# Performance work log

Measured on AMD Instinct MI355X. Metric: run time of the kernel, lower is better.

The kernel has to match this reference:

```python
import jax, jax.numpy as jnp
import numpy as np

N = 100000
E = 3200000
D_IN = 256
D_OUT = 256
K = 3


def setup_inputs() -> dict:
    key = jax.random.key(0)
    k1, k2, k3, k4, k5 = jax.random.split(key, 5)
    x = jax.random.normal(k1, (N, D_IN), dtype=jnp.float32)
    # xavier-uniform-ish weight
    lim = float(np.sqrt(6.0 / (D_IN + D_OUT)))
    weight = jax.random.uniform(k2, (D_IN, D_OUT), dtype=jnp.float32, minval=-lim, maxval=lim)
    bias = jnp.zeros((D_OUT,), dtype=jnp.float32)
    edge_weight = jax.random.uniform(k3, (E,), dtype=jnp.float32) / 32.0  # ~normalized adj values
    edge_row = jax.random.randint(k4, (E,), 0, N, dtype=jnp.int32)
    edge_col = jax.random.randint(k5, (E,), 0, N, dtype=jnp.int32)
    return {"x": x, "weight": weight, "bias": bias, "edge_weight": edge_weight,
            "edge_row": edge_row, "edge_col": edge_col}


def _spmm(edge_weight, edge_row, edge_col, support):
    # out[i] = sum_{e: row_e == i} w_e * support[col_e]
    msgs = edge_weight[:, None] * support[edge_col]  # [E, D]
    return jax.ops.segment_sum(msgs, edge_row, num_segments=N)


def reference(x, weight, bias, edge_weight, edge_row, edge_col):
    support = x @ weight            # [N, D_OUT]
    output = support
    for _ in range(K):
        support = _spmm(edge_weight, edge_row, edge_col, support)
        output = output + support
    return output + bias
```

## Files before the change

### kernel.cpp

```cpp
#include <hip/hip_runtime.h>

#define D 256
#define NB 196
#define RPB_SHIFT 9
#define CAP 20480
#define CHUNK 8192

typedef __attribute__((ext_vector_type(8))) short bf16x8;
typedef __attribute__((ext_vector_type(4))) float f32x4;
typedef __attribute__((ext_vector_type(2))) float f32x2;

__device__ __forceinline__ unsigned bf16rne(float f) {
    unsigned u = __float_as_uint(f);
    return (u + 0x7fffu + ((u >> 16) & 1u)) >> 16;
}
__device__ __forceinline__ unsigned char fp8enc(float f) {
    return (unsigned char)(__builtin_amdgcn_cvt_pk_fp8_f32(f, f, 0, false) & 0xFF);
}


__global__ __launch_bounds__(256) void cursor_init(int* __restrict__ g) {
    int t = threadIdx.x;
    g[t] = t * CAP;
}

__global__ __launch_bounds__(256) void partA(const int* __restrict__ erow,
                                             const int* __restrict__ ecol,
                                             const float* __restrict__ ew,
                                             int* __restrict__ gcur,
                                             int2* __restrict__ temp, int E) {
    __shared__ int2 rec[CHUNK];
    __shared__ unsigned char bkt[CHUNK];
    __shared__ int hist[256], sc[256], excl[256], cur[256], lbase[256];
    int t = threadIdx.x;
    int base = blockIdx.x * CHUNK;
    hist[t] = 0;
    __syncthreads();
    int rows[32];
    #pragma unroll
    for (int j = 0; j < 32; j++) {
        int e = base + t + 256 * j;
        rows[j] = (e < E) ? erow[e] : -1;
        if (rows[j] >= 0) atomicAdd(&hist[rows[j] >> RPB_SHIFT], 1);
    }
    __syncthreads();
    sc[t] = hist[t];
    __syncthreads();
    for (int off = 1; off < 256; off <<= 1) {
        int v = (t >= off) ? sc[t - off] : 0;
        __syncthreads();
        sc[t] += v;
        __syncthreads();
    }
    int ex = sc[t] - hist[t];
    excl[t] = ex;
    cur[t] = ex;
    lbase[t] = atomicAdd(&gcur[t], hist[t]);
    __syncthreads();
    int total = sc[255];
    #pragma unroll
    for (int j = 0; j < 32; j++) {
        if (rows[j] >= 0) {
            int e = base + t + 256 * j;
            int b = rows[j] >> RPB_SHIFT;
            int rl = rows[j] & 511;
            int p = atomicAdd(&cur[b], 1);
            int2 r;
            r.x = ecol[e] | (rl << 17);
            r.y = __float_as_int(ew[e]);
            rec[p] = r;
            bkt[p] = (unsigned char)b;
        }
    }
    __syncthreads();
    for (int i = t; i < total; i += 256) {
        int b = bkt[i];
        temp[(size_t)lbase[b] + (i - excl[b])] = rec[i];
    }
}

__global__ __launch_bounds__(256) void scanB(const int* __restrict__ gcur,
                                             int* __restrict__ bbase) {
    __shared__ int sc[256];
    int t = threadIdx.x;
    int c = (t < NB) ? (gcur[t] - t * CAP) : 0;
    sc[t] = c;
    __syncthreads();
    for (int off = 1; off < 256; off <<= 1) {
        int v = (t >= off) ? sc[t - off] : 0;
        __syncthreads();
        sc[t] += v;
        __syncthreads();
    }
    if (t < NB) bbase[t] = sc[t] - c;
}

__global__ __launch_bounds__(256) void partB(const int2* __restrict__ temp,
                                             const int* __restrict__ gcur,
                                             const int* __restrict__ bbase,
                                             int* __restrict__ row_ptr,
                                             int2* __restrict__ edges,
                                             int N, int E) {
    __shared__ int hist[512], excl[512], scp[256];
    int b = blockIdx.x;
    int t = threadIdx.x;
    int cnt = gcur[b] - b * CAP;
    int base = bbase[b];
    const int2* src = temp + (size_t)b * CAP;
    hist[t] = 0;
    hist[t + 256] = 0;
    __syncthreads();
    for (int i = t; i < cnt; i += 256)
        atomicAdd(&hist[(src[i].x >> 17) & 511], 1);
    __syncthreads();
    int v0 = hist[2 * t], v1 = hist[2 * t + 1];
    int ps = v0 + v1;
    scp[t] = ps;
    __syncthreads();
    for (int off = 1; off < 256; off <<= 1) {
        int v = (t >= off) ? scp[t - off] : 0;
        __syncthreads();
        scp[t] += v;
        __syncthreads();
    }
    int ep = scp[t] - ps;
    excl[2 * t] = ep;
    excl[2 * t + 1] = ep + v0;
    int r0 = (b << RPB_SHIFT) + 2 * t;
    if (r0 < N) row_ptr[r0] = base + ep;
    if (r0 + 1 < N) row_ptr[r0 + 1] = base + ep + v0;
    if (b == 0 && t == 0) row_ptr[N] = E;
    __syncthreads();
    for (int i = t; i < cnt; i += 256) {
        int2 r = src[i];
        int rl = (r.x >> 17) & 511;
        int p = base + atomicAdd(&excl[rl], 1);
        int2 o;
        o.x = r.x & 0x1FFFF;
        o.y = r.y;
        edges[p] = o;
    }
}

__global__ __launch_bounds__(256) void wconv_kernel(const float* __restrict__ w,
                                                    bf16x8* __restrict__ Wf) {
    int idx = blockIdx.x * 256 + threadIdx.x;
    int lane = idx & 63, g = idx >> 6;
    int h = g >> 6, r = g & 63;
    int ct = r >> 2, ks = (h << 2) | (r & 3);
    int q = lane >> 4, c = lane & 15;
    int n = ct * 16 + c;
    int k0 = ks * 32 + q * 8;
    bf16x8 bv;
    #pragma unroll
    for (int j = 0; j < 8; j++)
        bv[j] = (short)bf16rne(w[(size_t)(k0 + j) * D + n]);
    Wf[idx] = bv;
}

__global__ __launch_bounds__(512, 4) void gemm_kernel(const float* __restrict__ x,
                                                      const bf16x8* __restrict__ Wf,
                                                      const float* __restrict__ bias,
                                                      unsigned char* __restrict__ s0f8,
                                                      float* __restrict__ out, int N) {
    __shared__ bf16x8 Wl[4096];
    int t = threadIdx.x;
    int wid = t >> 6, lane = t & 63;
    int q = lane >> 4, c = lane & 15;
    int row0 = blockIdx.x * 128 + wid * 16;
    int rA = row0 + c;
    if (rA >= N) rA = N - 1;
    const float* xr = x + (size_t)rA * D + q * 8;

    f32x4 acc[16];
    #pragma unroll
    for (int ct = 0; ct < 16; ct++) acc[ct] = (f32x4){0.f, 0.f, 0.f, 0.f};

    for (int h = 0; h < 2; h++) {
        if (h) __syncthreads();
        #pragma unroll
        for (int k2 = 0; k2 < 8; k2++)
            Wl[k2 * 512 + t] = Wf[h * 4096 + k2 * 512 + t];
        __syncthreads();
        #pragma unroll
        for (int ks2 = 0; ks2 < 4; ks2++) {
            int ks = h * 4 + ks2;
            float4 p = *(const float4*)(xr + ks * 32);
            float4 r = *(const float4*)(xr + ks * 32 + 4);
            bf16x8 a;
            a[0] = (short)bf16rne(p.x); a[1] = (short)bf16rne(p.y);
            a[2] = (short)bf16rne(p.z); a[3] = (short)bf16rne(p.w);
            a[4] = (short)bf16rne(r.x); a[5] = (short)bf16rne(r.y);
            a[6] = (short)bf16rne(r.z); a[7] = (short)bf16rne(r.w);
            #pragma unroll
            for (int ct = 0; ct < 16; ct++) {
                bf16x8 bfrag = Wl[(ct * 4 + ks2) * 64 + lane];
                acc[ct] = __builtin_amdgcn_mfma_f32_16x16x32_bf16(a, bfrag, acc[ct], 0, 0, 0);
            }
        }
    }

    int rbase = row0 + q * 4;
    #pragma unroll
    for (int ct = 0; ct < 16; ct++) {
        int col = ct * 16 + c;
        float bv = bias[col];
        #pragma unroll
        for (int r = 0; r < 4; r++) {
            int rr = rbase + r;
            if (rr < N) {
                float v = acc[ct][r];
                size_t o = (size_t)rr * D + col;
                s0f8[o] = fp8enc(v);
                out[o] = v + bv;
            }
        }
    }
}

__global__ __launch_bounds__(256) void spmm_kernel(const uint2* __restrict__ S2,
                                                   const int* __restrict__ row_ptr,
                                                   const int2* __restrict__ edges,
                                                   uint2* __restrict__ Snext2, int N) {
    int wid = threadIdx.x >> 6;
    int lane = threadIdx.x & 63;
    int half = lane >> 5;
    int hl = lane & 31;
    int rowbase = (blockIdx.x * 4 + wid) * 2;
    if (rowbase >= N) return;
    int row = rowbase + half;
    bool rv = row < N;
    int e   = rv ? row_ptr[row] : 0;
    int end = rv ? row_ptr[row + 1] : 0;
    int len = end - e;
    int lmax = max(len, __shfl_xor(len, 32));
    int nb = (lmax + 7) >> 3;
    int safe = (end > 0) ? end - 1 : 0;

    float a0 = 0.f, a1 = 0.f, a2 = 0.f, a3 = 0.f;
    float a4 = 0.f, a5 = 0.f, a6 = 0.f, a7 = 0.f;

    for (int b = 0; b < nb; b++) {
        int2 ed[8];
        #pragma unroll
        for (int j = 0; j < 8; j++) {
            int idx = e + j;
            ed[j] = edges[idx < end ? idx : safe];
        }
        uint2 v[8];
        #pragma unroll
        for (int j = 0; j < 8; j++)
            v[j] = S2[(unsigned)ed[j].x * 32u + hl];
        #pragma unroll
        for (int j = 0; j < 8; j++) {
            float wj = (e + j < end) ? __int_as_float(ed[j].y) : 0.f;
            f32x2 l0 = __builtin_amdgcn_cvt_pk_f32_fp8(v[j].x, false);
            f32x2 h0 = __builtin_amdgcn_cvt_pk_f32_fp8(v[j].x, true);
            f32x2 l1 = __builtin_amdgcn_cvt_pk_f32_fp8(v[j].y, false);
            f32x2 h1 = __builtin_amdgcn_cvt_pk_f32_fp8(v[j].y, true);
            a0 += wj * l0.x; a1 += wj * l0.y; a2 += wj * h0.x; a3 += wj * h0.y;
            a4 += wj * l1.x; a5 += wj * l1.y; a6 += wj * h1.x; a7 += wj * h1.y;
        }
        e += 8;
    }
    if (rv) {
        unsigned s0 = (unsigned)__builtin_amdgcn_cvt_pk_fp8_f32(a0, a1, 0, false);
        s0 = (unsigned)__builtin_amdgcn_cvt_pk_fp8_f32(a2, a3, (int)s0, true);
        unsigned s1 = (unsigned)__builtin_amdgcn_cvt_pk_fp8_f32(a4, a5, 0, false);
        s1 = (unsigned)__builtin_amdgcn_cvt_pk_fp8_f32(a6, a7, (int)s1, true);
        uint2 o; o.x = s0; o.y = s1;
        Snext2[(size_t)row * 32 + hl] = o;
    }
}

__global__ __launch_bounds__(256) void combine_kernel(float4* __restrict__ out,
                                                      const unsigned int* __restrict__ S1,
                                                      const unsigned int* __restrict__ S2,
                                                      const unsigned int* __restrict__ S3,
                                                      int n4) {
    int i = blockIdx.x * 256 + threadIdx.x;
    if (i >= n4) return;
    unsigned u1 = S1[i], u2 = S2[i], u3 = S3[i];
    f32x2 l1 = __builtin_amdgcn_cvt_pk_f32_fp8(u1, false);
    f32x2 h1 = __builtin_amdgcn_cvt_pk_f32_fp8(u1, true);
    f32x2 l2 = __builtin_amdgcn_cvt_pk_f32_fp8(u2, false);
    f32x2 h2 = __builtin_amdgcn_cvt_pk_f32_fp8(u2, true);
    f32x2 l3 = __builtin_amdgcn_cvt_pk_f32_fp8(u3, false);
    f32x2 h3 = __builtin_amdgcn_cvt_pk_f32_fp8(u3, true);
    float4 o = out[i];
    o.x += l1.x + l2.x + l3.x;
    o.y += l1.y + l2.y + l3.y;
    o.z += h1.x + h2.x + h3.x;
    o.w += h1.y + h2.y + h3.y;
    out[i] = o;
}

extern "C" void kernel_launch(void* const* d_in, const int* in_sizes, int n_in,
                              void* d_out, int out_size, void* d_ws, size_t ws_size,
                              hipStream_t stream) {
    const float* x      = (const float*)d_in[0];
    const float* weight = (const float*)d_in[1];
    const float* bias   = (const float*)d_in[2];
    const float* ew     = (const float*)d_in[3];
    const int*   erow   = (const int*)d_in[4];
    const int*   ecol   = (const int*)d_in[5];
    float* out = (float*)d_out;
    int N = in_sizes[0] / D;
    int E = in_sizes[3];

    char* ws = (char*)d_ws;
    size_t off = 0;
    auto walloc = [&](size_t bytes) -> void* {
        void* p = ws + off;
        off += (bytes + 255) & ~255ULL;
        return p;
    };
    unsigned char* Sa = (unsigned char*)walloc((size_t)N * D);
    unsigned char* Sb = (unsigned char*)walloc((size_t)N * D);
    unsigned char* Sc = (unsigned char*)walloc((size_t)N * D);
    int*    row_ptr = (int*)walloc((size_t)(N + 1) * 4);
    int*    gcur    = (int*)walloc(256 * 4);
    int*    bbase   = (int*)walloc(256 * 4);
    bf16x8* Wf      = (bf16x8*)walloc(128 * 64 * 16);
    int2*   temp    = (int2*)walloc((size_t)NB * CAP * 8);
    int2*   edges   = (int2*)walloc((size_t)E * 8);

    cursor_init<<<1, 256, 0, stream>>>(gcur);
    int nchunks = (E + CHUNK - 1) / CHUNK;
    partA<<<nchunks, 256, 0, stream>>>(erow, ecol, ew, gcur, temp, E);
    scanB<<<1, 256, 0, stream>>>(gcur, bbase);
    partB<<<NB, 256, 0, stream>>>(temp, gcur, bbase, row_ptr, edges, N, E);

    wconv_kernel<<<32, 256, 0, stream>>>(weight, Wf);
    gemm_kernel<<<(N + 127) / 128, 512, 0, stream>>>(x, Wf, bias, Sa, out, N);

    int sb = (N + 7) / 8;
    spmm_kernel<<<sb, 256, 0, stream>>>((const uint2*)Sa, row_ptr, edges,
                                        (uint2*)Sb, N);
    spmm_kernel<<<sb, 256, 0, stream>>>((const uint2*)Sb, row_ptr, edges,
                                        (uint2*)Sc, N);
    spmm_kernel<<<sb, 256, 0, stream>>>((const uint2*)Sc, row_ptr, edges,
                                        (uint2*)Sa, N);

    int n4 = N * (D / 4);
    combine_kernel<<<(n4 + 255) / 256, 256, 0, stream>>>((float4*)out,
                                                         (const unsigned int*)Sb,
                                                         (const unsigned int*)Sc,
                                                         (const unsigned int*)Sa, n4);
}
```

Before: 727.1 us.

## Pad CSR rows to multiples of eight and prefetch edges in SpMM

Each row's edge segment is padded to a multiple of 8 with zero-weight dummy edges, using separate start and end arrays and per-bucket slack space. This removes the per-edge bounds checks and masking in the SpMM inner loop. Column indices are pre-shifted to byte offsets, the next batch of edges is prefetched while the current one is processed, packed f32x2 FMAs are used, and the launch bounds ask for higher occupancy. The cost is extra edge traffic from padding and a larger edge buffer. Each half-wave now loops over its own row length rather than the pair maximum, so the two halves of a wave can diverge.

Measured after the change: 700.7 us. -3.6%, faster.

```diff
diff --git a/kernel.cpp b/kernel.cpp
--- a/kernel.cpp
+++ b/kernel.cpp
@@ -5,6 +5,7 @@
 #define RPB_SHIFT 9
 #define CAP 20480
 #define CHUNK 8192
+#define PADSLACK 4096
 
 typedef __attribute__((ext_vector_type(8))) short bf16x8;
 typedef __attribute__((ext_vector_type(4))) float f32x4;
@@ -98,14 +99,15 @@
 __global__ __launch_bounds__(256) void partB(const int2* __restrict__ temp,
                                              const int* __restrict__ gcur,
                                              const int* __restrict__ bbase,
-                                             int* __restrict__ row_ptr,
+                                             int* __restrict__ rps,
+                                             int* __restrict__ rpe,
                                              int2* __restrict__ edges,
                                              int N, int E) {
-    __shared__ int hist[512], excl[512], scp[256];
+    __shared__ int hist[512], excl[512], pst[512], scp[256];
     int b = blockIdx.x;
     int t = threadIdx.x;
     int cnt = gcur[b] - b * CAP;
-    int base = bbase[b];
+    int base = bbase[b] + b * PADSLACK;
     const int2* src = temp + (size_t)b * CAP;
     hist[t] = 0;
     hist[t + 256] = 0;
@@ -114,7 +116,8 @@
         atomicAdd(&hist[(src[i].x >> 17) & 511], 1);
     __syncthreads();
     int v0 = hist[2 * t], v1 = hist[2 * t + 1];
-    int ps = v0 + v1;
+    int p0 = (v0 + 7) & ~7, p1 = (v1 + 7) & ~7;
+    int ps = p0 + p1;
     scp[t] = ps;
     __syncthreads();
     for (int off = 1; off < 256; off <<= 1) {
@@ -125,21 +128,29 @@
     }
     int ep = scp[t] - ps;
     excl[2 * t] = ep;
-    excl[2 * t + 1] = ep + v0;
+    excl[2 * t + 1] = ep + p0;
+    pst[2 * t] = ep;
+    pst[2 * t + 1] = ep + p0;
     int r0 = (b << RPB_SHIFT) + 2 * t;
-    if (r0 < N) row_ptr[r0] = base + ep;
-    if (r0 + 1 < N) row_ptr[r0 + 1] = base + ep + v0;
-    if (b == 0 && t == 0) row_ptr[N] = E;
+    if (r0 < N)     { rps[r0]     = base + ep;      rpe[r0]     = base + ep + p0; }
+    if (r0 + 1 < N) { rps[r0 + 1] = base + ep + p0; rpe[r0 + 1] = base + ep + p0 + p1; }
     __syncthreads();
     for (int i = t; i < cnt; i += 256) {
         int2 r = src[i];
         int rl = (r.x >> 17) & 511;
         int p = base + atomicAdd(&excl[rl], 1);
         int2 o;
-        o.x = r.x & 0x1FFFF;
+        o.x = (r.x & 0x1FFFF) << 8;
         o.y = r.y;
         edges[p] = o;
     }
+    __syncthreads();
+    int c0 = hist[2 * t];
+    int b0 = base + pst[2 * t];
+    for (int k = c0; k < p0; k++) edges[b0 + k] = make_int2(0, 0);
+    int c1 = hist[2 * t + 1];
+    int b1 = base + pst[2 * t + 1];
+    for (int k = c1; k < p1; k++) edges[b1 + k] = make_int2(0, 0);
 }
 
 __global__ __launch_bounds__(256) void wconv_kernel(const float* __restrict__ w,
@@ -218,10 +229,11 @@
     }
 }
 
-__global__ __launch_bounds__(256) void spmm_kernel(const uint2* __restrict__ S2,
-                                                   const int* __restrict__ row_ptr,
-                                                   const int2* __restrict__ edges,
-                                                   uint2* __restrict__ Snext2, int N) {
+__global__ __launch_bounds__(256, 8) void spmm_kernel(const uint2* __restrict__ S2,
+                                                      const int* __restrict__ rps,
+                                                      const int* __restrict__ rpe,
+                                                      const int2* __restrict__ edges,
+                                                      uint2* __restrict__ Snext2, int N) {
     int wid = threadIdx.x >> 6;
     int lane = threadIdx.x & 63;
     int half = lane >> 5;
@@ -230,44 +242,45 @@
     if (rowbase >= N) return;
     int row = rowbase + half;
     bool rv = row < N;
-    int e   = rv ? row_ptr[row] : 0;
-    int end = rv ? row_ptr[row + 1] : 0;
-    int len = end - e;
-    int lmax = max(len, __shfl_xor(len, 32));
-    int nb = (lmax + 7) >> 3;
-    int safe = (end > 0) ? end - 1 : 0;
-
-    float a0 = 0.f, a1 = 0.f, a2 = 0.f, a3 = 0.f;
-    float a4 = 0.f, a5 = 0.f, a6 = 0.f, a7 = 0.f;
-
-    for (int b = 0; b < nb; b++) {
-        int2 ed[8];
+    int e   = rv ? rps[row] : 0;
+    int end = rv ? rpe[row] : 0;
+    const char* Sb = (const char*)S2 + (hl << 3);
+
+    f32x2 acc0 = {0.f, 0.f}, acc1 = {0.f, 0.f}, acc2 = {0.f, 0.f}, acc3 = {0.f, 0.f};
+
+    int2 edn[8];
+    #pragma unroll
+    for (int j = 0; j < 8; j++) edn[j] = edges[e + j];
+
+    while (e < end) {
+        uint2 v[8];
+        #pragma unroll
+        for (int j = 0; j < 8; j++)
+            v[j] = *(const uint2*)(Sb + (unsigned)edn[j].x);
+        float w[8];
+        #pragma unroll
+        for (int j = 0; j < 8; j++) w[j] = __int_as_float(edn[j].y);
+        #pragma unroll
+        for (int j = 0; j < 8; j++) edn[j] = edges[e + 8 + j];
         #pragma unroll
         for (int j = 0; j < 8; j++) {
-            int idx = e + j;
-            ed[j] = edges[idx < end ? idx : safe];
-        }
-        uint2 v[8];
-        #pragma unroll
-        for (int j = 0; j < 8; j++)
-            v[j] = S2[(unsigned)ed[j].x * 32u + hl];
-        #pragma unroll
-        for (int j = 0; j < 8; j++) {
-            float wj = (e + j < end) ? __int_as_float(ed[j].y) : 0.f;
+            f32x2 w2 = {w[j], w[j]};
             f32x2 l0 = __builtin_amdgcn_cvt_pk_f32_fp8(v[j].x, false);
             f32x2 h0 = __builtin_amdgcn_cvt_pk_f32_fp8(v[j].x, true);
             f32x2 l1 = __builtin_amdgcn_cvt_pk_f32_fp8(v[j].y, false);
             f32x2 h1 = __builtin_amdgcn_cvt_pk_f32_fp8(v[j].y, true);
-            a0 += wj * l0.x; a1 += wj * l0.y; a2 += wj * h0.x; a3 += wj * h0.y;
-            a4 += wj * l1.x; a5 += wj * l1.y; a6 += wj * h1.x; a7 += wj * h1.y;
+            acc0 += w2 * l0;
+            acc1 += w2 * h0;
+            acc2 += w2 * l1;
+            acc3 += w2 * h1;
         }
         e += 8;
     }
     if (rv) {
-        unsigned s0 = (unsigned)__builtin_amdgcn_cvt_pk_fp8_f32(a0, a1, 0, false);
-        s0 = (unsigned)__builtin_amdgcn_cvt_pk_fp8_f32(a2, a3, (int)s0, true);
-        unsigned s1 = (unsigned)__builtin_amdgcn_cvt_pk_fp8_f32(a4, a5, 0, false);
-        s1 = (unsigned)__builtin_amdgcn_cvt_pk_fp8_f32(a6, a7, (int)s1, true);
+        unsigned s0 = (unsigned)__builtin_amdgcn_cvt_pk_fp8_f32(acc0.x, acc0.y, 0, false);
+        s0 = (unsigned)__builtin_amdgcn_cvt_pk_fp8_f32(acc1.x, acc1.y, (int)s0, true);
+        unsigned s1 = (unsigned)__builtin_amdgcn_cvt_pk_fp8_f32(acc2.x, acc2.y, 0, false);
+        s1 = (unsigned)__builtin_amdgcn_cvt_pk_fp8_f32(acc3.x, acc3.y, (int)s1, true);
         uint2 o; o.x = s0; o.y = s1;
         Snext2[(size_t)row * 32 + hl] = o;
     }
@@ -318,28 +331,29 @@
     unsigned char* Sa = (unsigned char*)walloc((size_t)N * D);
     unsigned char* Sb = (unsigned char*)walloc((size_t)N * D);
     unsigned char* Sc = (unsigned char*)walloc((size_t)N * D);
-    int*    row_ptr = (int*)walloc((size_t)(N + 1) * 4);
+    int*    rps     = (int*)walloc((size_t)N * 4);
+    int*    rpe     = (int*)walloc((size_t)N * 4);
     int*    gcur    = (int*)walloc(256 * 4);
     int*    bbase   = (int*)walloc(256 * 4);
     bf16x8* Wf      = (bf16x8*)walloc(128 * 64 * 16);
     int2*   temp    = (int2*)walloc((size_t)NB * CAP * 8);
-    int2*   edges   = (int2*)walloc((size_t)E * 8);
+    int2*   edges   = (int2*)walloc(((size_t)E + (size_t)NB * PADSLACK + 64) * 8);
 
     cursor_init<<<1, 256, 0, stream>>>(gcur);
     int nchunks = (E + CHUNK - 1) / CHUNK;
     partA<<<nchunks, 256, 0, stream>>>(erow, ecol, ew, gcur, temp, E);
     scanB<<<1, 256, 0, stream>>>(gcur, bbase);
-    partB<<<NB, 256, 0, stream>>>(temp, gcur, bbase, row_ptr, edges, N, E);
+    partB<<<NB, 256, 0, stream>>>(temp, gcur, bbase, rps, rpe, edges, N, E);
 
     wconv_kernel<<<32, 256, 0, stream>>>(weight, Wf);
     gemm_kernel<<<(N + 127) / 128, 512, 0, stream>>>(x, Wf, bias, Sa, out, N);
 
     int sb = (N + 7) / 8;
-    spmm_kernel<<<sb, 256, 0, stream>>>((const uint2*)Sa, row_ptr, edges,
+    spmm_kernel<<<sb, 256, 0, stream>>>((const uint2*)Sa, rps, rpe, edges,
                                         (uint2*)Sb, N);
-    spmm_kernel<<<sb, 256, 0, stream>>>((const uint2*)Sb, row_ptr, edges,
+    spmm_kernel<<<sb, 256, 0, stream>>>((const uint2*)Sb, rps, rpe, edges,
                                         (uint2*)Sc, N);
-    spmm_kernel<<<sb, 256, 0, stream>>>((const uint2*)Sc, row_ptr, edges,
+    spmm_kernel<<<sb, 256, 0, stream>>>((const uint2*)Sc, rps, rpe, edges,
                                         (uint2*)Sa, N);
 
     int n4 = N * (D / 4);
```
